# Kernel tuning notes

Hardware: AMD Instinct MI355X
Metric: run time of the kernel (lower is better)

The kernel has to match this reference:

```python
import jax, jax.numpy as jnp
import numpy as np

# Config: AydinConfig(hidden_dim=1024, intermediate_dim=2048, num_experts=8, top_k=2)
E, H, I, K = 8, 1024, 2048, 2
B, S = 4, 2048


def setup_inputs() -> dict:
    key = jax.random.key(0)
    k1, k2, k3, k4 = jax.random.split(key, 4)
    x = jax.random.normal(k1, (B, S, H), dtype=jnp.float32)
    # nn.Linear(H, E, bias=False): weight shape (E, H), default init ~ U(-1/sqrt(H), 1/sqrt(H))
    router_w = jax.random.uniform(k2, (E, H), dtype=jnp.float32,
                                  minval=-1.0, maxval=1.0) / np.sqrt(H).astype(np.float32)
    # normal init, std=0.02 (reset_parameters)
    w13 = jax.random.normal(k3, (E, H, 2 * I), dtype=jnp.float32) * 0.02
    w2 = jax.random.normal(k4, (E, I, H), dtype=jnp.float32) * 0.02
    return {"x": x, "router_w": router_w, "w13": w13, "w2": w2}


def reference(x, router_w, w13, w2):
    # Router: logits (B,S,E) -> softmax -> top-k with renormalized weights
    logits = jnp.einsum('bsh,eh->bse', x, router_w)
    probs = jax.nn.softmax(logits, axis=-1)
    weights, indices = jax.lax.top_k(probs, K)            # (B,S,K)
    weights = weights / (weights.sum(axis=-1, keepdims=True) + 1e-6)
    # Expert SwiGLU, computed densely over all experts then gathered.
    # Same math as the torch per-token weight gather, but avoids the
    # (B,S,K,H,2I) gathered-weight blowup.
    h13 = jnp.einsum('bsh,ehi->bsei', x, w13)             # (B,S,E,2I)
    gate, up = jnp.split(h13, 2, axis=-1)                 # (B,S,E,I) each
    h = jax.nn.silu(gate) * up
    y = jnp.einsum('bsei,eih->bseh', h, w2)               # (B,S,E,H)
    # Gather top-k expert outputs and combine with routing weights
    y_sel = jnp.take_along_axis(y, indices[..., None], axis=2)  # (B,S,K,H)
    return (y_sel * weights[..., None]).sum(axis=2)       # (B,S,H)
```

## Files before the change

### kernel.cpp

```cpp
#include <hip/hip_runtime.h>
#include <hip/hip_bf16.h>
#include <math.h>

#define NEXP 8
#define HD 1024
#define ID 2048
#define NTOK 8192
#define NROWS 16384

typedef __bf16 bf16_t;
typedef __bf16 bf16x8 __attribute__((ext_vector_type(8)));
typedef float f32x4 __attribute__((ext_vector_type(4)));

#define BK 32
#define MAXT1 72
#define MAXT2 136

__device__ __forceinline__ void gl16(const void* g, void* l) {
    __builtin_amdgcn_global_load_lds(
        (const __attribute__((address_space(1))) unsigned int*)g,
        (__attribute__((address_space(3))) unsigned int*)l, 16, 0, 0);
}

__global__ __launch_bounds__(256)
void router_kernel(const float* __restrict__ x, const float* __restrict__ rw,
                   bf16_t* __restrict__ xb, int* __restrict__ topk_idx,
                   float* __restrict__ topk_w)
{
    const int t = blockIdx.x;
    const int tid = threadIdx.x;
    const float4 xv = ((const float4*)(x + (size_t)t * HD))[tid];
    float acc[NEXP];
#pragma unroll
    for (int e = 0; e < NEXP; ++e) {
        const float4 w4 = ((const float4*)(rw + e * HD))[tid];
        acc[e] = xv.x * w4.x + xv.y * w4.y + xv.z * w4.z + xv.w * w4.w;
    }
    bf16_t tmp[4] = {(bf16_t)xv.x, (bf16_t)xv.y, (bf16_t)xv.z, (bf16_t)xv.w};
    *(uint2*)(xb + (size_t)t * HD + tid * 4) = *(const uint2*)tmp;

    __shared__ float red[4][NEXP];
    const int lane = tid & 63, wv = tid >> 6;
#pragma unroll
    for (int e = 0; e < NEXP; ++e) {
        float v = acc[e];
#pragma unroll
        for (int off = 32; off >= 1; off >>= 1) v += __shfl_down(v, off, 64);
        if (lane == 0) red[wv][e] = v;
    }
    __syncthreads();
    if (tid == 0) {
        float lg[NEXP], mx = -1e30f;
#pragma unroll
        for (int e = 0; e < NEXP; ++e) {
            lg[e] = red[0][e] + red[1][e] + red[2][e] + red[3][e];
            mx = fmaxf(mx, lg[e]);
        }
        float p[NEXP], s = 0.f;
#pragma unroll
        for (int e = 0; e < NEXP; ++e) { p[e] = __expf(lg[e] - mx); s += p[e]; }
        const float inv = 1.f / s;
#pragma unroll
        for (int e = 0; e < NEXP; ++e) p[e] *= inv;
        int i0 = 0; float p0 = p[0];
#pragma unroll
        for (int e = 1; e < NEXP; ++e) if (p[e] > p0) { p0 = p[e]; i0 = e; }
        int i1 = -1; float p1 = -1.f;
#pragma unroll
        for (int e = 0; e < NEXP; ++e) if (e != i0 && p[e] > p1) { p1 = p[e]; i1 = e; }
        const float d = 1.f / (p0 + p1 + 1e-6f);
        topk_idx[t * 2 + 0] = i0; topk_idx[t * 2 + 1] = i1;
        topk_w[t * 2 + 0] = p0 * d; topk_w[t * 2 + 1] = p1 * d;
    }
}

__global__ __launch_bounds__(256)
void count_kernel(const int* __restrict__ topk_idx, int* __restrict__ counts)
{
    __shared__ int lc[NEXP];
    const int tid = threadIdx.x;
    if (tid < NEXP) lc[tid] = 0;
    __syncthreads();
    const int t = blockIdx.x * 256 + tid;
    atomicAdd(&lc[topk_idx[t * 2 + 0]], 1);
    atomicAdd(&lc[topk_idx[t * 2 + 1]], 1);
    __syncthreads();
    if (tid < NEXP) atomicAdd(&counts[tid], lc[tid]);
}

__global__ void scan_kernel(const int* __restrict__ counts, int* __restrict__ offsets,
                            int* __restrict__ cursor,
                            unsigned* __restrict__ map256, unsigned* __restrict__ map128)
{
    __shared__ int tb2[NEXP + 1], tb1[NEXP + 1];
    if (threadIdx.x == 0) {
        int s = 0, t2 = 0, t1 = 0;
        for (int e = 0; e < NEXP; ++e) {
            offsets[e] = s; cursor[e] = s; s += counts[e];
            tb2[e] = t2; t2 += (counts[e] + 255) >> 8;
            tb1[e] = t1; t1 += (counts[e] + 127) >> 7;
        }
        tb2[NEXP] = t2; tb1[NEXP] = t1;
    }
    __syncthreads();
    for (int i = threadIdx.x; i < MAXT1; i += 64) {
        unsigned v = 0xFFFFFFFFu;
#pragma unroll
        for (int e = 0; e < NEXP; ++e)
            if (i >= tb2[e] && i < tb2[e + 1]) v = ((unsigned)e << 16) | (unsigned)(i - tb2[e]);
        map256[i] = v;
    }
    for (int i = threadIdx.x; i < MAXT2; i += 64) {
        unsigned v = 0xFFFFFFFFu;
#pragma unroll
        for (int e = 0; e < NEXP; ++e)
            if (i >= tb1[e] && i < tb1[e + 1]) v = ((unsigned)e << 16) | (unsigned)(i - tb1[e]);
        map128[i] = v;
    }
}

__global__ __launch_bounds__(256)
void scatter_kernel(const int* __restrict__ topk_idx, const float* __restrict__ topk_w,
                    int* __restrict__ cursor, int* __restrict__ token_list,
                    float* __restrict__ row_w, int* __restrict__ row_pos)
{
    __shared__ int lc[NEXP], gbase[NEXP];
    const int tid = threadIdx.x;
    if (tid < NEXP) lc[tid] = 0;
    __syncthreads();
    const int t = blockIdx.x * 256 + tid;
    const int e0 = topk_idx[t * 2 + 0], e1 = topk_idx[t * 2 + 1];
    const int lp0 = atomicAdd(&lc[e0], 1);
    const int lp1 = atomicAdd(&lc[e1], 1);
    __syncthreads();
    if (tid < NEXP) gbase[tid] = atomicAdd(&cursor[tid], lc[tid]);
    __syncthreads();
    const int p0 = gbase[e0] + lp0, p1 = gbase[e1] + lp1;
    token_list[p0] = t; row_w[p0] = topk_w[t * 2 + 0]; row_pos[t * 2 + 0] = p0;
    token_list[p1] = t; row_w[p1] = topk_w[t * 2 + 1]; row_pos[t * 2 + 1] = p1;
}

__global__ __launch_bounds__(256)
void precast_kernel(const float* __restrict__ src, bf16_t* __restrict__ dst,
                    int K, int N)
{
    const int e = blockIdx.z;
    src += (size_t)e * K * N;
    dst += (size_t)e * K * N;
    const int n0 = blockIdx.x * 64, k0 = blockIdx.y * 64;
    __shared__ float tile[64][65];
    const int tid = threadIdx.x;
    const int tx = (tid & 15) * 4, ty = tid >> 4;
#pragma unroll
    for (int p = 0; p < 4; ++p) {
        const float4 v = *(const float4*)(src + (size_t)(k0 + ty + p * 16) * N + n0 + tx);
        tile[ty + p * 16][tx + 0] = v.x;
        tile[ty + p * 16][tx + 1] = v.y;
        tile[ty + p * 16][tx + 2] = v.z;
        tile[ty + p * 16][tx + 3] = v.w;
    }
    __syncthreads();
    const int n = tid >> 2, kc = (tid & 3) * 16;
    bf16_t outv[16];
#pragma unroll
    for (int j = 0; j < 16; ++j) outv[j] = (bf16_t)tile[kc + j][n];
    bf16_t* d = dst + (size_t)(n0 + n) * K + k0 + kc;
    *(uint4*)d = *(uint4*)outv;
    *(uint4*)(d + 8) = *((uint4*)outv + 1);
}

__global__ __launch_bounds__(256)
void precast13_kernel(const float* __restrict__ src, bf16_t* __restrict__ dst)
{
    const int e = blockIdx.z;
    src += (size_t)e * HD * (2 * ID);
    dst += (size_t)e * HD * (2 * ID);
    const int g = blockIdx.x;
    const int k0 = blockIdx.y * 64;
    __shared__ float tile[64][65];
    const int tid = threadIdx.x;
    const int tx = (tid & 7) * 4, ty = tid >> 3;
#pragma unroll
    for (int s = 0; s < 2; ++s) {
        const int cbase = s == 0 ? g * 32 : 2048 + g * 32;
#pragma unroll
        for (int p = 0; p < 2; ++p) {
            const int kk = ty + p * 32;
            const float4 v = *(const float4*)(src + (size_t)(k0 + kk) * (2 * ID) + cbase + tx);
            tile[kk][s * 32 + tx + 0] = v.x;
            tile[kk][s * 32 + tx + 1] = v.y;
            tile[kk][s * 32 + tx + 2] = v.z;
            tile[kk][s * 32 + tx + 3] = v.w;
        }
    }
    __syncthreads();
    const int m = tid >> 2, kc = (tid & 3) * 16;
    bf16_t outv[16];
#pragma unroll
    for (int j = 0; j < 16; ++j) outv[j] = (bf16_t)tile[kc + j][m];
    bf16_t* d = dst + (size_t)(g * 64 + m) * HD + k0 + kc;
    *(uint4*)d = *(uint4*)outv;
    *(uint4*)(d + 8) = *((uint4*)outv + 1);
}

__global__ __launch_bounds__(512, 2)
void gemm1_kernel(const bf16_t* __restrict__ xb, const bf16_t* __restrict__ w13i,
                  const int* __restrict__ offsets, const int* __restrict__ counts,
                  const int* __restrict__ token_list,
                  const unsigned* __restrict__ tile_map, bf16_t* __restrict__ hbuf)
{
    const unsigned tm = tile_map[blockIdx.y];
    if (tm == 0xFFFFFFFFu) return;
    const int e = (int)(tm >> 16), mt = (int)(tm & 0xFFFFu);
    const int rows = counts[e];
    const int row_base = offsets[e];
    const int r0 = mt * 256;
    const int N0 = blockIdx.x * 256;

    __shared__ alignas(16) bf16_t As[2][256][32];
    __shared__ alignas(16) bf16_t Bs[2][256][32];

    const int tid = threadIdx.x;
    const int lane = tid & 63, wv = tid >> 6;
    const int wr = wv >> 2, wc = wv & 3;
    const int ln15 = lane & 15, q = lane >> 4;
    const int cs = (q ^ ((ln15 >> 1) & 3)) * 8;

    const int srow = tid >> 2;
    const int schunk = ((tid & 3) ^ ((tid >> 3) & 3)) * 8;
    int gr0 = row_base + r0 + srow;       if (gr0 > NROWS - 1) gr0 = NROWS - 1;
    int gr1 = row_base + r0 + 128 + srow; if (gr1 > NROWS - 1) gr1 = NROWS - 1;
    const bf16_t* a0 = xb + (size_t)token_list[gr0] * HD + schunk;
    const bf16_t* a1 = xb + (size_t)token_list[gr1] * HD + schunk;
    const bf16_t* b0 = w13i + ((size_t)e * (2 * ID) + N0 + srow) * HD + schunk;
    const bf16_t* b1 = b0 + (size_t)128 * HD;

    f32x4 acc[8][4];
#pragma unroll
    for (int i = 0; i < 8; ++i)
#pragma unroll
        for (int j = 0; j < 4; ++j)
#pragma unroll
            for (int c = 0; c < 4; ++c) acc[i][j][c] = 0.f;

    gl16(a0, &As[0][0][0] + tid * 8);
    gl16(a1, &As[0][128][0] + tid * 8);
    gl16(b0, &Bs[0][0][0] + tid * 8);
    gl16(b1, &Bs[0][128][0] + tid * 8);
    __syncthreads();

    const int NT = HD / BK;
    int cur = 0;
    for (int t = 0; t < NT; ++t) {
        if (t + 1 < NT) {
            const int k = (t + 1) * BK;
            const int nb = cur ^ 1;
            gl16(a0 + k, &As[nb][0][0] + tid * 8);
            gl16(a1 + k, &As[nb][128][0] + tid * 8);
            gl16(b0 + k, &Bs[nb][0][0] + tid * 8);
            gl16(b1 + k, &Bs[nb][128][0] + tid * 8);
        }
        bf16x8 af[8], bfr[4];
#pragma unroll
        for (int i = 0; i < 8; ++i)
            af[i] = *(const bf16x8*)&As[cur][wr * 128 + i * 16 + ln15][cs];
#pragma unroll
        for (int j = 0; j < 4; ++j)
            bfr[j] = *(const bf16x8*)&Bs[cur][wc * 64 + j * 16 + ln15][cs];
        __builtin_amdgcn_s_setprio(1);
#pragma unroll
        for (int i = 0; i < 8; ++i)
#pragma unroll
            for (int j = 0; j < 4; ++j)
                acc[i][j] = __builtin_amdgcn_mfma_f32_16x16x32_bf16(af[i], bfr[j], acc[i][j], 0, 0, 0);
        __builtin_amdgcn_s_setprio(0);
        __syncthreads();
        cur ^= 1;
    }

    const int hbase = (N0 >> 1) + wc * 32;
#pragma unroll
    for (int i = 0; i < 8; ++i) {
#pragma unroll
        for (int reg = 0; reg < 4; ++reg) {
            const int rr = wr * 128 + i * 16 + q * 4 + reg;
            if (r0 + rr < rows) {
                bf16_t* dst = hbuf + (size_t)(row_base + r0 + rr) * ID + hbase + ln15;
#pragma unroll
                for (int j = 0; j < 2; ++j) {
                    const float g = acc[i][j][reg], u = acc[i][j + 2][reg];
                    dst[j * 16] = (bf16_t)((g / (1.f + __expf(-g))) * u);
                }
            }
        }
    }
}

__global__ __launch_bounds__(512, 2)
void gemm2_kernel(const bf16_t* __restrict__ hbuf, const bf16_t* __restrict__ w2b,
                  const int* __restrict__ offsets, const int* __restrict__ counts,
                  const float* __restrict__ row_w,
                  const unsigned* __restrict__ tile_map, float* __restrict__ ybuf)
{
    const unsigned tm = tile_map[blockIdx.y];
    if (tm == 0xFFFFFFFFu) return;
    const int e = (int)(tm >> 16), mt = (int)(tm & 0xFFFFu);
    const int rows = counts[e];
    const int row_base = offsets[e];
    const int r0 = mt * 128;
    const int N0 = blockIdx.x * 256;

    __shared__ alignas(16) bf16_t As[2][128][32];
    __shared__ alignas(16) bf16_t Bs[2][256][32];
    __shared__ float rww_s[128];

    const int tid = threadIdx.x;
    if (tid < 128) {
        int gr = row_base + r0 + tid; if (gr > NROWS - 1) gr = NROWS - 1;
        rww_s[tid] = row_w[gr];
    }
    const int lane = tid & 63, wv = tid >> 6;
    const int wr = wv >> 2, wc = wv & 3;
    const int ln15 = lane & 15, q = lane >> 4;
    const int cs = (q ^ ((ln15 >> 1) & 3)) * 8;

    const int srow = tid >> 2;
    const int schunk = ((tid & 3) ^ ((tid >> 3) & 3)) * 8;
    int gr0 = row_base + r0 + srow; if (gr0 > NROWS - 1) gr0 = NROWS - 1;
    const bf16_t* a0 = hbuf + (size_t)gr0 * ID + schunk;
    const bf16_t* b0 = w2b + ((size_t)e * HD + N0 + srow) * ID + schunk;
    const bf16_t* b1 = b0 + (size_t)128 * ID;

    f32x4 acc[4][4];
#pragma unroll
    for (int i = 0; i < 4; ++i)
#pragma unroll
        for (int j = 0; j < 4; ++j)
#pragma unroll
            for (int c = 0; c < 4; ++c) acc[i][j][c] = 0.f;

    gl16(a0, &As[0][0][0] + tid * 8);
    gl16(b0, &Bs[0][0][0] + tid * 8);
    gl16(b1, &Bs[0][128][0] + tid * 8);
    __syncthreads();

    const int NT = ID / BK;
    int cur = 0;
    for (int t = 0; t < NT; ++t) {
        if (t + 1 < NT) {
            const int k = (t + 1) * BK;
            const int nb = cur ^ 1;
            gl16(a0 + k, &As[nb][0][0] + tid * 8);
            gl16(b0 + k, &Bs[nb][0][0] + tid * 8);
            gl16(b1 + k, &Bs[nb][128][0] + tid * 8);
        }
        bf16x8 af[4], bfr[4];
#pragma unroll
        for (int i = 0; i < 4; ++i)
            af[i] = *(const bf16x8*)&As[cur][wr * 64 + i * 16 + ln15][cs];
#pragma unroll
        for (int j = 0; j < 4; ++j)
            bfr[j] = *(const bf16x8*)&Bs[cur][wc * 64 + j * 16 + ln15][cs];
        __builtin_amdgcn_s_setprio(1);
#pragma unroll
        for (int i = 0; i < 4; ++i)
#pragma unroll
            for (int j = 0; j < 4; ++j)
                acc[i][j] = __builtin_amdgcn_mfma_f32_16x16x32_bf16(af[i], bfr[j], acc[i][j], 0, 0, 0);
        __builtin_amdgcn_s_setprio(0);
        __syncthreads();
        cur ^= 1;
    }

#pragma unroll
    for (int i = 0; i < 4; ++i) {
#pragma unroll
        for (int reg = 0; reg < 4; ++reg) {
            const int rr = wr * 64 + i * 16 + q * 4 + reg;
            if (r0 + rr < rows) {
                const float w = rww_s[rr];
                float* dst = ybuf + (size_t)(row_base + r0 + rr) * HD + N0 + wc * 64 + ln15;
#pragma unroll
                for (int j = 0; j < 4; ++j)
                    dst[j * 16] = acc[i][j][reg] * w;
            }
        }
    }
}

__global__ __launch_bounds__(256)
void combine_kernel(const float* __restrict__ ybuf, const int* __restrict__ row_pos,
                    float* __restrict__ out)
{
    const int t = blockIdx.x;
    const int p0 = row_pos[t * 2 + 0], p1 = row_pos[t * 2 + 1];
    const float4 a = ((const float4*)(ybuf + (size_t)p0 * HD))[threadIdx.x];
    const float4 b = ((const float4*)(ybuf + (size_t)p1 * HD))[threadIdx.x];
    float4 o; o.x = a.x + b.x; o.y = a.y + b.y; o.z = a.z + b.z; o.w = a.w + b.w;
    ((float4*)(out + (size_t)t * HD))[threadIdx.x] = o;
}

extern "C" void kernel_launch(void* const* d_in, const int* in_sizes, int n_in,
                              void* d_out, int out_size, void* d_ws, size_t ws_size,
                              hipStream_t stream) {
    const float* x   = (const float*)d_in[0];
    const float* rw  = (const float*)d_in[1];
    const float* w13 = (const float*)d_in[2];
    const float* w2  = (const float*)d_in[3];
    float* out = (float*)d_out;

    char* ws = (char*)d_ws;
    int*      counts     = (int*)(ws + 0);
    int*      cursor     = (int*)(ws + 64);
    int*      offsets    = (int*)(ws + 128);
    int*      topk_idx   = (int*)(ws + 256);
    float*    topk_w     = (float*)(ws + 256 + 1 * 65536);
    int*      token_list = (int*)(ws + 256 + 2 * 65536);
    float*    row_w      = (float*)(ws + 256 + 3 * 65536);
    int*      row_pos    = (int*)(ws + 256 + 4 * 65536);
    unsigned* map256     = (unsigned*)(ws + 256 + 5 * 65536);
    unsigned* map128     = (unsigned*)(ws + 256 + 6 * 65536);
    const size_t MB = 1024 * 1024;
    bf16_t* xb   = (bf16_t*)(ws + 1 * MB);
    bf16_t* hbuf = (bf16_t*)(ws + 17 * MB);
    bf16_t* w13i = (bf16_t*)(ws + 81 * MB);
    float*  ybuf = (float*)(ws + 81 * MB);
    bf16_t* w2b  = (bf16_t*)(ws + 145 * MB);

    hipMemsetAsync(ws, 0, 256, stream);

    dim3 gp1(64, HD / 64, NEXP);
    precast13_kernel<<<gp1, 256, 0, stream>>>(w13, w13i);
    dim3 gp2(HD / 64, ID / 64, NEXP);
    precast_kernel<<<gp2, 256, 0, stream>>>(w2, w2b, ID, HD);

    router_kernel<<<NTOK, 256, 0, stream>>>(x, rw, xb, topk_idx, topk_w);
    count_kernel<<<NTOK / 256, 256, 0, stream>>>(topk_idx, counts);
    scan_kernel<<<1, 64, 0, stream>>>(counts, offsets, cursor, map256, map128);
    scatter_kernel<<<NTOK / 256, 256, 0, stream>>>(topk_idx, topk_w, cursor,
                                                   token_list, row_w, row_pos);

    dim3 g1(2 * ID / 256, MAXT1);
    gemm1_kernel<<<g1, 512, 0, stream>>>(xb, w13i, offsets, counts, token_list,
                                         map256, hbuf);
    dim3 g2(HD / 256, MAXT2);
    gemm2_kernel<<<g2, 512, 0, stream>>>(hbuf, w2b, offsets, counts, row_w,
                                         map128, ybuf);
    combine_kernel<<<NTOK, 256, 0, stream>>>(ybuf, row_pos, out);
}
```

Baseline: 647.2 us.

## Deepen GEMM pipelines to 4-stage LDS ring with vmcnt-based waits

Both expert GEMM kernels move from double-buffered LDS to a 4-slot ring with three tiles prefetched ahead. Each step waits with an explicit s_waitcnt vmcnt on only the oldest outstanding loads, then issues one barrier, replacing the full __syncthreads after every K tile. The aim is to hide global-memory latency better and remove one barrier per iteration. The cost is doubled LDS use: gemm1 grows from 64KB to 128KB and gemm2 from about 48KB to 96KB. That may cut the 2-blocks-per-CU occupancy declared in launch_bounds, and the hand-written vmcnt counts must match the number of loads in flight.

```diff
diff --git a/kernel.cpp b/kernel.cpp
--- a/kernel.cpp
+++ b/kernel.cpp
@@ -217,8 +217,8 @@
     const int r0 = mt * 256;
     const int N0 = blockIdx.x * 256;
 
-    __shared__ alignas(16) bf16_t As[2][256][32];
-    __shared__ alignas(16) bf16_t Bs[2][256][32];
+    __shared__ alignas(16) bf16_t As[4][256][32];
+    __shared__ alignas(16) bf16_t Bs[4][256][32];
 
     const int tid = threadIdx.x;
     const int lane = tid & 63, wv = tid >> 6;
@@ -243,40 +243,44 @@
 #pragma unroll
             for (int c = 0; c < 4; ++c) acc[i][j][c] = 0.f;
 
-    gl16(a0, &As[0][0][0] + tid * 8);
-    gl16(a1, &As[0][128][0] + tid * 8);
-    gl16(b0, &Bs[0][0][0] + tid * 8);
-    gl16(b1, &Bs[0][128][0] + tid * 8);
-    __syncthreads();
-
-    const int NT = HD / BK;
-    int cur = 0;
-    for (int t = 0; t < NT; ++t) {
-        if (t + 1 < NT) {
-            const int k = (t + 1) * BK;
-            const int nb = cur ^ 1;
-            gl16(a0 + k, &As[nb][0][0] + tid * 8);
-            gl16(a1 + k, &As[nb][128][0] + tid * 8);
-            gl16(b0 + k, &Bs[nb][0][0] + tid * 8);
-            gl16(b1 + k, &Bs[nb][128][0] + tid * 8);
-        }
-        bf16x8 af[8], bfr[4];
-#pragma unroll
-        for (int i = 0; i < 8; ++i)
-            af[i] = *(const bf16x8*)&As[cur][wr * 128 + i * 16 + ln15][cs];
-#pragma unroll
-        for (int j = 0; j < 4; ++j)
-            bfr[j] = *(const bf16x8*)&Bs[cur][wc * 64 + j * 16 + ln15][cs];
-        __builtin_amdgcn_s_setprio(1);
-#pragma unroll
-        for (int i = 0; i < 8; ++i)
-#pragma unroll
-            for (int j = 0; j < 4; ++j)
-                acc[i][j] = __builtin_amdgcn_mfma_f32_16x16x32_bf16(af[i], bfr[j], acc[i][j], 0, 0, 0);
-        __builtin_amdgcn_s_setprio(0);
-        __syncthreads();
-        cur ^= 1;
-    }
+#define G1_STAGE(s, kt) do { \
+    const int kk_ = (kt) * BK; \
+    gl16(a0 + kk_, &As[s][0][0]   + tid * 8); \
+    gl16(a1 + kk_, &As[s][128][0] + tid * 8); \
+    gl16(b0 + kk_, &Bs[s][0][0]   + tid * 8); \
+    gl16(b1 + kk_, &Bs[s][128][0] + tid * 8); \
+} while (0)
+
+#define G1_STEP(kt, VMSTR, PF) do { \
+    asm volatile("s_waitcnt vmcnt(" VMSTR ")" ::: "memory"); \
+    __builtin_amdgcn_s_barrier(); \
+    asm volatile("" ::: "memory"); \
+    if (PF) G1_STAGE(((kt) + 3) & 3, (kt) + 3); \
+    const int sl_ = (kt) & 3; \
+    bf16x8 af[8], bfr[4]; \
+    _Pragma("unroll") \
+    for (int i_ = 0; i_ < 8; ++i_) \
+        af[i_] = *(const bf16x8*)&As[sl_][wr * 128 + i_ * 16 + ln15][cs]; \
+    _Pragma("unroll") \
+    for (int j_ = 0; j_ < 4; ++j_) \
+        bfr[j_] = *(const bf16x8*)&Bs[sl_][wc * 64 + j_ * 16 + ln15][cs]; \
+    __builtin_amdgcn_s_setprio(1); \
+    _Pragma("unroll") \
+    for (int i_ = 0; i_ < 8; ++i_) \
+        _Pragma("unroll") \
+        for (int j_ = 0; j_ < 4; ++j_) \
+            acc[i_][j_] = __builtin_amdgcn_mfma_f32_16x16x32_bf16(af[i_], bfr[j_], acc[i_][j_], 0, 0, 0); \
+    __builtin_amdgcn_s_setprio(0); \
+} while (0)
+
+    G1_STAGE(0, 0); G1_STAGE(1, 1); G1_STAGE(2, 2);
+    const int NKT = HD / BK;
+    for (int kt = 0; kt < NKT - 3; ++kt) G1_STEP(kt, "8", true);
+    G1_STEP(NKT - 3, "8", false);
+    G1_STEP(NKT - 2, "4", false);
+    G1_STEP(NKT - 1, "0", false);
+#undef G1_STEP
+#undef G1_STAGE
 
     const int hbase = (N0 >> 1) + wc * 32;
 #pragma unroll
@@ -310,8 +314,8 @@
     const int r0 = mt * 128;
     const int N0 = blockIdx.x * 256;
 
-    __shared__ alignas(16) bf16_t As[2][128][32];
-    __shared__ alignas(16) bf16_t Bs[2][256][32];
+    __shared__ alignas(16) bf16_t As[4][128][32];
+    __shared__ alignas(16) bf16_t Bs[4][256][32];
     __shared__ float rww_s[128];
 
     const int tid = threadIdx.x;
@@ -339,38 +343,43 @@
 #pragma unroll
             for (int c = 0; c < 4; ++c) acc[i][j][c] = 0.f;
 
-    gl16(a0, &As[0][0][0] + tid * 8);
-    gl16(b0, &Bs[0][0][0] + tid * 8);
-    gl16(b1, &Bs[0][128][0] + tid * 8);
-    __syncthreads();
-
-    const int NT = ID / BK;
-    int cur = 0;
-    for (int t = 0; t < NT; ++t) {
-        if (t + 1 < NT) {
-            const int k = (t + 1) * BK;
-            const int nb = cur ^ 1;
-            gl16(a0 + k, &As[nb][0][0] + tid * 8);
-            gl16(b0 + k, &Bs[nb][0][0] + tid * 8);
-            gl16(b1 + k, &Bs[nb][128][0] + tid * 8);
-        }
-        bf16x8 af[4], bfr[4];
-#pragma unroll
-        for (int i = 0; i < 4; ++i)
-            af[i] = *(const bf16x8*)&As[cur][wr * 64 + i * 16 + ln15][cs];
-#pragma unroll
-        for (int j = 0; j < 4; ++j)
-            bfr[j] = *(const bf16x8*)&Bs[cur][wc * 64 + j * 16 + ln15][cs];
-        __builtin_amdgcn_s_setprio(1);
-#pragma unroll
-        for (int i = 0; i < 4; ++i)
-#pragma unroll
-            for (int j = 0; j < 4; ++j)
-                acc[i][j] = __builtin_amdgcn_mfma_f32_16x16x32_bf16(af[i], bfr[j], acc[i][j], 0, 0, 0);
-        __builtin_amdgcn_s_setprio(0);
-        __syncthreads();
-        cur ^= 1;
-    }
+#define G2_STAGE(s, kt) do { \
+    const int kk_ = (kt) * BK; \
+    gl16(a0 + kk_, &As[s][0][0]   + tid * 8); \
+    gl16(b0 + kk_, &Bs[s][0][0]   + tid * 8); \
+    gl16(b1 + kk_, &Bs[s][128][0] + tid * 8); \
+} while (0)
+
+#define G2_STEP(kt, VMSTR, PF) do { \
+    asm volatile("s_waitcnt vmcnt(" VMSTR ")" ::: "memory"); \
+    __builtin_amdgcn_s_barrier(); \
+    asm volatile("" ::: "memory"); \
+    if (PF) G2_STAGE(((kt) + 3) & 3, (kt) + 3); \
+    const int sl_ = (kt) & 3; \
+    bf16x8 af[4], bfr[4]; \
+    _Pragma("unroll") \
+    for (int i_ = 0; i_ < 4; ++i_) \
+        af[i_] = *(const bf16x8*)&As[sl_][wr * 64 + i_ * 16 + ln15][cs]; \
+    _Pragma("unroll") \
+    for (int j_ = 0; j_ < 4; ++j_) \
+        bfr[j_] = *(const bf16x8*)&Bs[sl_][wc * 64 + j_ * 16 + ln15][cs]; \
+    __builtin_amdgcn_s_setprio(1); \
+    _Pragma("unroll") \
+    for (int i_ = 0; i_ < 4; ++i_) \
+        _Pragma("unroll") \
+        for (int j_ = 0; j_ < 4; ++j_) \
+            acc[i_][j_] = __builtin_amdgcn_mfma_f32_16x16x32_bf16(af[i_], bfr[j_], acc[i_][j_], 0, 0, 0); \
+    __builtin_amdgcn_s_setprio(0); \
+} while (0)
+
+    G2_STAGE(0, 0); G2_STAGE(1, 1); G2_STAGE(2, 2);
+    const int NKT = ID / BK;
+    for (int kt = 0; kt < NKT - 3; ++kt) G2_STEP(kt, "6", true);
+    G2_STEP(NKT - 3, "6", false);
+    G2_STEP(NKT - 2, "3", false);
+    G2_STEP(NKT - 1, "0", false);
+#undef G2_STEP
+#undef G2_STAGE
 
 #pragma unroll
     for (int i = 0; i < 4; ++i) {
```

New measurement: 686.4 us. 6.0% more time.
